# Kernel tuning notes

Hardware: AMD Instinct MI355X
Metric: run time of the kernel (lower is better)

The kernel has to match this reference:

```python
import jax, jax.numpy as jnp
import numpy as np

B = 4096          # number of sessions
MEAN_LEN = 50     # mean items per session
N = B * MEAN_LEN  # total items (ragged lengths sum to this)
H = 256           # feat_input_dim == context_input_dim == hidden_dim


def setup_inputs() -> dict:
    key = jax.random.key(0)
    k1, k2, k3, k4, k5, k6, k7 = jax.random.split(key, 7)
    # ragged lengths in [20, 80] adjusted so they sum exactly to N
    rng = np.random.default_rng(0)
    lens = rng.integers(20, 81, size=B)
    lens = (lens * (N / lens.sum())).astype(np.int64)
    lens[-1] += N - lens.sum()
    s = 1.0 / np.sqrt(H)
    return {
        "feats": jax.random.normal(k1, (N, H), jnp.float32),
        "feat_context": jax.random.normal(k2, (N, H), jnp.float32),
        "batch_num_items": jnp.asarray(lens, jnp.int64),
        "Wu": jax.random.uniform(k3, (H, H), jnp.float32, -s, s),
        "bu": jax.random.uniform(k4, (H,), jnp.float32, -s, s),
        "Wv": jax.random.uniform(k5, (H, H), jnp.float32, -s, s),
        "We": jax.random.uniform(k6, (H,), jnp.float32, -s, s),
        "Wout": jax.random.uniform(k7, (H, H), jnp.float32, -s, s),
    }


def reference(feats, feat_context, batch_num_items, Wu, bu, Wv, We, Wout):
    n = feats.shape[0]
    b = batch_num_items.shape[0]
    # additive attention score per item
    feat_u = feats @ Wu.T + bu                     # [N, H]
    feat_v = feat_context @ Wv.T                   # [N, H]
    e = jax.nn.sigmoid(feat_u + feat_v) @ We       # [N]
    # segment ids from ragged lengths (static total length => jit-safe)
    seg = jnp.repeat(jnp.arange(b), batch_num_items, total_repeat_length=n)
    # segment softmax (numerically stable)
    m = jax.ops.segment_max(e, seg, num_segments=b)        # [B]
    ex = jnp.exp(e - m[seg])                               # [N]
    denom = jax.ops.segment_sum(ex, seg, num_segments=b)   # [B]
    alpha = ex / denom[seg]                                # [N]
    # weighted segment-sum pooling
    rst = jax.ops.segment_sum(feats * alpha[:, None], seg, num_segments=b)  # [B, H]
    return rst @ Wout.T
```

## Files before the change

### kernel.cpp

```cpp
#include <hip/hip_runtime.h>
#include <hip/hip_bf16.h>
#include <cstdint>
#include <cstddef>

#define H 256
#define CHUNK 128

typedef __attribute__((ext_vector_type(8))) short    frag8;
typedef __attribute__((ext_vector_type(4))) float    f32x4;
typedef __attribute__((ext_vector_type(4))) uint32_t u32x4;
typedef __attribute__((ext_vector_type(8))) unsigned short ushort8;

__device__ __forceinline__ unsigned short f32_to_bf16(float f) {
    uint32_t u = __float_as_uint(f);
    u = (u + 0x7FFFu + ((u >> 16) & 1u)) >> 16;
    return (unsigned short)u;
}

__device__ __forceinline__ uint32_t pk_bf16(float a, float b) {
    union { __hip_bfloat162 h2; uint32_t u; } cv;
    cv.h2 = __float22bfloat162_rn(make_float2(a, b));
    return cv.u;
}

__global__ void prep(const float* __restrict__ Wu, const float* __restrict__ Wv,
                     const float* __restrict__ Wout,
                     unsigned short* __restrict__ Wopt, float* __restrict__ WoutT) {
    int bid = blockIdx.x, tid = threadIdx.x;
    if (bid < 64) {
        int idx  = bid * 256 + tid;
        int lane = idx & 63;
        int ct   = (idx >> 6) & 15;
        int ksg  = idx >> 10;
        int col  = ct * 16 + (lane & 15);
        int kg   = ksg * 32 + (lane >> 4) * 8;
        ushort8 pk;
        #pragma unroll
        for (int j = 0; j < 8; j++) {
            int k = kg + j;
            float v = (k < 256) ? Wu[col * 256 + k] : Wv[col * 256 + (k - 256)];
            pk[j] = f32_to_bf16(v);
        }
        *(ushort8*)&Wopt[(size_t)idx * 8] = pk;
    } else {
        int t2 = (bid - 64) * 256 + tid;
        int j = t2 & 255, k = t2 >> 8;
        WoutT[t2] = Wout[j * 256 + k];
    }
}

__global__ void seg_offsets(const int* __restrict__ lens, int B, int* __restrict__ off,
                            int2* __restrict__ chunks, int* __restrict__ chunk_cnt) {
    __shared__ int partL[256], partC[256];
    int tid = threadIdx.x;
    bool is64 = (B >= 3) && (lens[1] == 0) && (lens[3] == 0) && (lens[5] == 0);
    int per = (B + 255) / 256;
    int base = tid * per;
    int sL = 0, sC = 0;
    for (int i = 0; i < per; i++) {
        int idx = base + i;
        if (idx < B) {
            int l = is64 ? lens[2 * idx] : lens[idx];
            sL += l;
            sC += (l + CHUNK - 1) / CHUNK;
        }
    }
    partL[tid] = sL; partC[tid] = sC;
    __syncthreads();
    for (int d = 1; d < 256; d <<= 1) {
        int vL = partL[tid], vC = partC[tid];
        int aL = (tid >= d) ? partL[tid - d] : 0;
        int aC = (tid >= d) ? partC[tid - d] : 0;
        __syncthreads();
        partL[tid] = vL + aL; partC[tid] = vC + aC;
        __syncthreads();
    }
    int runL = partL[tid] - sL;
    int runC = partC[tid] - sC;
    for (int i = 0; i < per; i++) {
        int idx = base + i;
        if (idx < B) {
            int l = is64 ? lens[2 * idx] : lens[idx];
            off[idx] = runL;
            int n = (l + CHUNK - 1) / CHUNK;
            for (int c = 0; c < n; c++)
                chunks[runC + c] = make_int2(idx, runL + c * CHUNK);
            runC += n;
            runL += l;
        }
    }
    if (tid == 255) { off[B] = partL[255]; chunk_cnt[0] = partC[255]; }
}

__global__ __launch_bounds__(512, 4) void fused_e(
        const float* __restrict__ feats, const float* __restrict__ ctx,
        const unsigned short* __restrict__ Wopt,
        const float* __restrict__ bu, const float* __restrict__ We,
        float* __restrict__ e_out) {
    __shared__ unsigned short a_lds[64 * 128];
    __shared__ float e_part[8 * 64];

    const int tid  = threadIdx.x;
    const int lane = tid & 63;
    const int w    = tid >> 6;
    const int l15  = lane & 15;
    const int q    = lane >> 4;
    const size_t m0 = (size_t)blockIdx.x * 64;
    const int r0   = tid >> 3;
    const int c8   = tid & 7;
    const int swz  = r0 & 15;

    f32x4 acc[4][2];
    #pragma unroll
    for (int i = 0; i < 4; i++)
        #pragma unroll
        for (int j = 0; j < 2; j++)
            acc[i][j] = (f32x4)(0.0f);

    f32x4 pre[4];
    {
        const float* p = feats + (m0 + r0) * H + c8 * 16;
        pre[0] = *(const f32x4*)p;       pre[1] = *(const f32x4*)(p + 4);
        pre[2] = *(const f32x4*)(p + 8); pre[3] = *(const f32x4*)(p + 12);
    }

    #pragma unroll
    for (int kt = 0; kt < 4; ++kt) {
        u32x4 g0, g1;
        g0[0] = pk_bf16(pre[0][0], pre[0][1]); g0[1] = pk_bf16(pre[0][2], pre[0][3]);
        g0[2] = pk_bf16(pre[1][0], pre[1][1]); g0[3] = pk_bf16(pre[1][2], pre[1][3]);
        g1[0] = pk_bf16(pre[2][0], pre[2][1]); g1[1] = pk_bf16(pre[2][2], pre[2][3]);
        g1[2] = pk_bf16(pre[3][0], pre[3][1]); g1[3] = pk_bf16(pre[3][2], pre[3][3]);

        __syncthreads();
        *(u32x4*)&a_lds[r0 * 128 + (((2 * c8    ) ^ swz) * 8)] = g0;
        *(u32x4*)&a_lds[r0 * 128 + (((2 * c8 + 1) ^ swz) * 8)] = g1;
        __syncthreads();

        frag8 bfr[4][2];
        #pragma unroll
        for (int ks = 0; ks < 4; ++ks)
            #pragma unroll
            for (int ci = 0; ci < 2; ++ci)
                bfr[ks][ci] = *(const frag8*)&Wopt[
                    (((size_t)(kt * 4 + ks) * 16 + (w * 2 + ci)) * 64 + lane) * 8];
        __builtin_amdgcn_sched_barrier(0);

        if (kt < 3) {
            const float* src = (kt + 1 < 2) ? feats : ctx;
            const int kb = ((kt + 1) & 1) * 128;
            const float* p = src + (m0 + r0) * H + kb + c8 * 16;
            pre[0] = *(const f32x4*)p;       pre[1] = *(const f32x4*)(p + 4);
            pre[2] = *(const f32x4*)(p + 8); pre[3] = *(const f32x4*)(p + 12);
        }

        #pragma unroll
        for (int ks = 0; ks < 4; ++ks) {
            frag8 afr[4];
            #pragma unroll
            for (int rt = 0; rt < 4; ++rt)
                afr[rt] = *(const frag8*)&a_lds[(rt * 16 + l15) * 128 + (((ks * 4 + q) ^ l15) * 8)];
            #pragma unroll
            for (int rt = 0; rt < 4; ++rt)
                #pragma unroll
                for (int ci = 0; ci < 2; ++ci)
                    acc[rt][ci] = __builtin_amdgcn_mfma_f32_16x16x32_bf16(
                        afr[rt], bfr[ks][ci], acc[rt][ci], 0, 0, 0);
        }
    }

    float buv[2], wev[2];
    #pragma unroll
    for (int ci = 0; ci < 2; ++ci) {
        int col = w * 32 + ci * 16 + l15;
        buv[ci] = bu[col];
        wev[ci] = We[col];
    }
    #pragma unroll
    for (int rt = 0; rt < 4; ++rt) {
        #pragma unroll
        for (int r = 0; r < 4; ++r) {
            float s = 0.0f;
            #pragma unroll
            for (int ci = 0; ci < 2; ++ci) {
                float h = acc[rt][ci][r] + buv[ci];
                s += wev[ci] * __builtin_amdgcn_rcpf(1.0f + __expf(-h));
            }
            s += __shfl_xor(s, 1, 64);
            s += __shfl_xor(s, 2, 64);
            s += __shfl_xor(s, 4, 64);
            s += __shfl_xor(s, 8, 64);
            if (l15 == 0) e_part[w * 64 + rt * 16 + q * 4 + r] = s;
        }
    }
    __syncthreads();
    if (tid < 64) {
        float s = 0.0f;
        #pragma unroll
        for (int ww = 0; ww < 8; ++ww) s += e_part[ww * 64 + tid];
        e_out[m0 + tid] = s;
    }
}

__global__ __launch_bounds__(256) void seg_stats(
        float* __restrict__ e, const int* __restrict__ off, int B) {
    int seg = blockIdx.x * 4 + (threadIdx.x >> 6);
    int lane = threadIdx.x & 63;
    if (seg >= B) return;
    int start = off[seg];
    int len = off[seg + 1] - start;
    float m = -3.0e38f;
    for (int i = lane; i < len; i += 64) m = fmaxf(m, e[start + i]);
    #pragma unroll
    for (int o = 32; o > 0; o >>= 1) m = fmaxf(m, __shfl_xor(m, o, 64));
    float s = 0.0f;
    for (int i = lane; i < len; i += 64) s += __expf(e[start + i] - m);
    #pragma unroll
    for (int o = 32; o > 0; o >>= 1) s += __shfl_xor(s, o, 64);
    float inv = (s > 0.0f) ? 1.0f / s : 0.0f;
    for (int i = lane; i < len; i += 64) e[start + i] = __expf(e[start + i] - m) * inv;
}

__global__ __launch_bounds__(256) void pool_chunks(
        const float* __restrict__ alpha, const float* __restrict__ feats,
        const int* __restrict__ off, const int2* __restrict__ chunks,
        const int* __restrict__ chunk_cnt, float* __restrict__ rst) {
    __shared__ float redf[4 * 256];
    int idx = blockIdx.x;
    if (idx >= chunk_cnt[0]) return;
    int2 en = chunks[idx];
    int seg = en.x, cstart = en.y;
    int sstart = off[seg], send = off[seg + 1];
    int clen = send - cstart;
    if (clen > CHUNK) clen = CHUNK;
    int tid = threadIdx.x, lane = tid & 63, g = tid >> 6;

    const f32x4* F = (const f32x4*)feats + (size_t)cstart * 64 + lane;
    const float* A = alpha + cstart;
    f32x4 acc0 = (f32x4)(0.0f), acc1 = (f32x4)(0.0f);
    int i = g;
    for (; i + 4 < clen; i += 8) {
        acc0 += A[i]     * F[(size_t)i * 64];
        acc1 += A[i + 4] * F[(size_t)(i + 4) * 64];
    }
    if (i < clen) acc0 += A[i] * F[(size_t)i * 64];
    acc0 += acc1;
    *(f32x4*)&redf[g * 256 + lane * 4] = acc0;
    __syncthreads();
    float v = redf[tid] + redf[256 + tid] + redf[512 + tid] + redf[768 + tid];
    if (send - sstart > CHUNK) atomicAdd(&rst[(size_t)seg * H + tid], v);
    else rst[(size_t)seg * H + tid] = v;
}

#define RB 8
__global__ __launch_bounds__(256) void out_gemm(
        const float* __restrict__ rst, const float* __restrict__ WoutT,
        float* __restrict__ out) {
    __shared__ float r[RB * 256];
    const int tid = threadIdx.x;
    const size_t b0 = (size_t)blockIdx.x * RB;
    for (int i = tid; i < RB * 256; i += 256) r[i] = rst[b0 * 256 + i];
    __syncthreads();
    float acc[RB];
    #pragma unroll
    for (int j = 0; j < RB; j++) acc[j] = 0.0f;
    for (int k = 0; k < 256; k += 4) {
        f32x4 rw[RB];
        #pragma unroll
        for (int j = 0; j < RB; j++) rw[j] = *(const f32x4*)&r[j * 256 + k];
        #pragma unroll
        for (int kk = 0; kk < 4; kk++) {
            float wv = WoutT[(size_t)(k + kk) * 256 + tid];
            #pragma unroll
            for (int j = 0; j < RB; j++) acc[j] += rw[j][kk] * wv;
        }
    }
    #pragma unroll
    for (int j = 0; j < RB; j++) out[(b0 + j) * 256 + tid] = acc[j];
}

extern "C" void kernel_launch(void* const* d_in, const int* in_sizes, int n_in,
                              void* d_out, int out_size, void* d_ws, size_t ws_size,
                              hipStream_t stream) {
    const float* feats = (const float*)d_in[0];
    const float* ctx   = (const float*)d_in[1];
    const int*   lens  = (const int*)d_in[2];
    const float* Wu    = (const float*)d_in[3];
    const float* bu    = (const float*)d_in[4];
    const float* Wv    = (const float*)d_in[5];
    const float* We    = (const float*)d_in[6];
    const float* Wout  = (const float*)d_in[7];
    float* out = (float*)d_out;

    const int N = in_sizes[0] / H;
    const int B = in_sizes[2];
    const int maxChunks = B + (N + CHUNK - 1) / CHUNK;

    char* w = (char*)d_ws;
    auto carve = [&](size_t bytes) {
        char* p = w;
        w += (bytes + 255) & ~(size_t)255;
        return p;
    };
    int*            off    = (int*)           carve((size_t)(B + 1) * sizeof(int));
    float*          e      = (float*)         carve((size_t)N * sizeof(float));
    float*          rst    = (float*)         carve((size_t)B * H * sizeof(float));
    unsigned short* Wopt   = (unsigned short*)carve((size_t)16 * 16 * 64 * 8 * sizeof(unsigned short));
    float*          WoutT  = (float*)         carve((size_t)H * H * sizeof(float));
    int2*           chunks = (int2*)          carve((size_t)maxChunks * sizeof(int2));
    int*            ccnt   = (int*)           carve(sizeof(int));

    hipMemsetAsync(rst, 0, (size_t)B * H * sizeof(float), stream);

    prep        <<<320,         256, 0, stream>>>(Wu, Wv, Wout, Wopt, WoutT);
    seg_offsets <<<1,           256, 0, stream>>>(lens, B, off, chunks, ccnt);
    fused_e     <<<N / 64,      512, 0, stream>>>(feats, ctx, Wopt, bu, We, e);
    seg_stats   <<<(B + 3) / 4, 256, 0, stream>>>(e, off, B);
    pool_chunks <<<maxChunks,   256, 0, stream>>>(e, feats, off, chunks, ccnt, rst);
    out_gemm    <<<B / RB,      256, 0, stream>>>(rst, WoutT, out);
}
```

Measured before the change: 525.4 us.

## Persistent double-buffered fused_e kernel and fuse segment softmax into pooling

Measured after the change: 583.7 us. 11.1% more time.

```diff
diff --git a/kernel.cpp b/kernel.cpp
--- a/kernel.cpp
+++ b/kernel.cpp
@@ -96,8 +96,8 @@
         const float* __restrict__ feats, const float* __restrict__ ctx,
         const unsigned short* __restrict__ Wopt,
         const float* __restrict__ bu, const float* __restrict__ We,
-        float* __restrict__ e_out) {
-    __shared__ unsigned short a_lds[64 * 128];
+        float* __restrict__ e_out, int nTiles) {
+    __shared__ unsigned short a_lds[2][64 * 128];
     __shared__ float e_part[8 * 64];
 
     const int tid  = threadIdx.x;
@@ -105,10 +105,20 @@
     const int w    = tid >> 6;
     const int l15  = lane & 15;
     const int q    = lane >> 4;
-    const size_t m0 = (size_t)blockIdx.x * 64;
     const int r0   = tid >> 3;
     const int c8   = tid & 7;
     const int swz  = r0 & 15;
+    const int G    = gridDim.x;
+
+    if (blockIdx.x >= nTiles) return;
+
+    float buv[2], wev[2];
+    #pragma unroll
+    for (int ci = 0; ci < 2; ++ci) {
+        int col = w * 32 + ci * 16 + l15;
+        buv[ci] = bu[col];
+        wev[ci] = We[col];
+    }
 
     f32x4 acc[4][2];
     #pragma unroll
@@ -118,87 +128,90 @@
             acc[i][j] = (f32x4)(0.0f);
 
     f32x4 pre[4];
-    {
-        const float* p = feats + (m0 + r0) * H + c8 * 16;
+    auto loadA = [&](int tile, int kt) {
+        const float* s = (kt < 2) ? feats : ctx;
+        const float* p = s + ((size_t)tile * 64 + r0) * H + ((kt & 1) << 7) + (c8 << 4);
         pre[0] = *(const f32x4*)p;       pre[1] = *(const f32x4*)(p + 4);
         pre[2] = *(const f32x4*)(p + 8); pre[3] = *(const f32x4*)(p + 12);
-    }
-
-    #pragma unroll
-    for (int kt = 0; kt < 4; ++kt) {
+    };
+    auto cvt_store = [&](int buf) {
         u32x4 g0, g1;
         g0[0] = pk_bf16(pre[0][0], pre[0][1]); g0[1] = pk_bf16(pre[0][2], pre[0][3]);
         g0[2] = pk_bf16(pre[1][0], pre[1][1]); g0[3] = pk_bf16(pre[1][2], pre[1][3]);
         g1[0] = pk_bf16(pre[2][0], pre[2][1]); g1[1] = pk_bf16(pre[2][2], pre[2][3]);
         g1[2] = pk_bf16(pre[3][0], pre[3][1]); g1[3] = pk_bf16(pre[3][2], pre[3][3]);
-
-        __syncthreads();
-        *(u32x4*)&a_lds[r0 * 128 + (((2 * c8    ) ^ swz) * 8)] = g0;
-        *(u32x4*)&a_lds[r0 * 128 + (((2 * c8 + 1) ^ swz) * 8)] = g1;
-        __syncthreads();
-
-        frag8 bfr[4][2];
-        #pragma unroll
-        for (int ks = 0; ks < 4; ++ks)
-            #pragma unroll
-            for (int ci = 0; ci < 2; ++ci)
-                bfr[ks][ci] = *(const frag8*)&Wopt[
-                    (((size_t)(kt * 4 + ks) * 16 + (w * 2 + ci)) * 64 + lane) * 8];
-        __builtin_amdgcn_sched_barrier(0);
-
-        if (kt < 3) {
-            const float* src = (kt + 1 < 2) ? feats : ctx;
-            const int kb = ((kt + 1) & 1) * 128;
-            const float* p = src + (m0 + r0) * H + kb + c8 * 16;
-            pre[0] = *(const f32x4*)p;       pre[1] = *(const f32x4*)(p + 4);
-            pre[2] = *(const f32x4*)(p + 8); pre[3] = *(const f32x4*)(p + 12);
-        }
-
-        #pragma unroll
-        for (int ks = 0; ks < 4; ++ks) {
-            frag8 afr[4];
-            #pragma unroll
-            for (int rt = 0; rt < 4; ++rt)
-                afr[rt] = *(const frag8*)&a_lds[(rt * 16 + l15) * 128 + (((ks * 4 + q) ^ l15) * 8)];
-            #pragma unroll
-            for (int rt = 0; rt < 4; ++rt)
+        *(u32x4*)&a_lds[buf][r0 * 128 + (((2 * c8    ) ^ swz) * 8)] = g0;
+        *(u32x4*)&a_lds[buf][r0 * 128 + (((2 * c8 + 1) ^ swz) * 8)] = g1;
+    };
+
+    loadA(blockIdx.x, 0);
+    cvt_store(0);
+    loadA(blockIdx.x, 1);
+    __syncthreads();
+
+    int cur = 0;
+    for (int tile = blockIdx.x; tile < nTiles; tile += G) {
+        #pragma unroll
+        for (int kt = 0; kt < 4; ++kt) {
+            frag8 bfr[4][2];
+            #pragma unroll
+            for (int ks = 0; ks < 4; ++ks)
                 #pragma unroll
                 for (int ci = 0; ci < 2; ++ci)
-                    acc[rt][ci] = __builtin_amdgcn_mfma_f32_16x16x32_bf16(
-                        afr[rt], bfr[ks][ci], acc[rt][ci], 0, 0, 0);
-        }
-    }
-
-    float buv[2], wev[2];
-    #pragma unroll
-    for (int ci = 0; ci < 2; ++ci) {
-        int col = w * 32 + ci * 16 + l15;
-        buv[ci] = bu[col];
-        wev[ci] = We[col];
-    }
-    #pragma unroll
-    for (int rt = 0; rt < 4; ++rt) {
-        #pragma unroll
-        for (int r = 0; r < 4; ++r) {
+                    bfr[ks][ci] = *(const frag8*)&Wopt[
+                        (((size_t)(kt * 4 + ks) * 16 + (w * 2 + ci)) * 64 + lane) * 8];
+
+            #pragma unroll
+            for (int ks = 0; ks < 4; ++ks) {
+                frag8 afr[4];
+                #pragma unroll
+                for (int rt = 0; rt < 4; ++rt)
+                    afr[rt] = *(const frag8*)&a_lds[cur][(rt * 16 + l15) * 128 + (((ks * 4 + q) ^ l15) * 8)];
+                #pragma unroll
+                for (int rt = 0; rt < 4; ++rt)
+                    #pragma unroll
+                    for (int ci = 0; ci < 2; ++ci)
+                        acc[rt][ci] = __builtin_amdgcn_mfma_f32_16x16x32_bf16(
+                            afr[rt], bfr[ks][ci], acc[rt][ci], 0, 0, 0);
+            }
+
+            const bool last_step = (kt == 3) && (tile + G >= nTiles);
+            if (!last_step) {
+                cvt_store(cur ^ 1);
+                int kt2 = kt + 2, tile2 = tile;
+                if (kt2 >= 4) { kt2 -= 4; tile2 += G; }
+                if (tile2 < nTiles) loadA(tile2, kt2);
+            }
+            cur ^= 1;
+            __syncthreads();
+        }
+
+        #pragma unroll
+        for (int rt = 0; rt < 4; ++rt) {
+            #pragma unroll
+            for (int r = 0; r < 4; ++r) {
+                float s = 0.0f;
+                #pragma unroll
+                for (int ci = 0; ci < 2; ++ci) {
+                    float h = acc[rt][ci][r] + buv[ci];
+                    s += wev[ci] * __builtin_amdgcn_rcpf(1.0f + __expf(-h));
+                    acc[rt][ci][r] = 0.0f;
+                }
+                s += __shfl_xor(s, 1, 64);
+                s += __shfl_xor(s, 2, 64);
+                s += __shfl_xor(s, 4, 64);
+                s += __shfl_xor(s, 8, 64);
+                if (l15 == 0) e_part[w * 64 + rt * 16 + q * 4 + r] = s;
+            }
+        }
+        __syncthreads();
+        if (tid < 64) {
             float s = 0.0f;
             #pragma unroll
-            for (int ci = 0; ci < 2; ++ci) {
-                float h = acc[rt][ci][r] + buv[ci];
-                s += wev[ci] * __builtin_amdgcn_rcpf(1.0f + __expf(-h));
-            }
-            s += __shfl_xor(s, 1, 64);
-            s += __shfl_xor(s, 2, 64);
-            s += __shfl_xor(s, 4, 64);
-            s += __shfl_xor(s, 8, 64);
-            if (l15 == 0) e_part[w * 64 + rt * 16 + q * 4 + r] = s;
-        }
-    }
-    __syncthreads();
-    if (tid < 64) {
-        float s = 0.0f;
-        #pragma unroll
-        for (int ww = 0; ww < 8; ++ww) s += e_part[ww * 64 + tid];
-        e_out[m0 + tid] = s;
+            for (int ww = 0; ww < 8; ++ww) s += e_part[ww * 64 + tid];
+            e_out[(size_t)tile * 64 + tid] = s;
+        }
+        __syncthreads();
     }
 }
 
@@ -209,6 +222,7 @@
     if (seg >= B) return;
     int start = off[seg];
     int len = off[seg + 1] - start;
+    if (len <= CHUNK) return;
     float m = -3.0e38f;
     for (int i = lane; i < len; i += 64) m = fmaxf(m, e[start + i]);
     #pragma unroll
@@ -222,10 +236,11 @@
 }
 
 __global__ __launch_bounds__(256) void pool_chunks(
-        const float* __restrict__ alpha, const float* __restrict__ feats,
+        const float* __restrict__ ealpha, const float* __restrict__ feats,
         const int* __restrict__ off, const int2* __restrict__ chunks,
         const int* __restrict__ chunk_cnt, float* __restrict__ rst) {
     __shared__ float redf[4 * 256];
+    __shared__ float smred[8];
     int idx = blockIdx.x;
     if (idx >= chunk_cnt[0]) return;
     int2 en = chunks[idx];
@@ -234,21 +249,45 @@
     int clen = send - cstart;
     if (clen > CHUNK) clen = CHUNK;
     int tid = threadIdx.x, lane = tid & 63, g = tid >> 6;
+    const bool multi = (send - sstart) > CHUNK;
+
+    float m = 0.0f, inv = 1.0f;
+    if (!multi) {
+        float v = (tid < clen) ? ealpha[cstart + tid] : -3.0e38f;
+        #pragma unroll
+        for (int o = 32; o > 0; o >>= 1) v = fmaxf(v, __shfl_xor(v, o, 64));
+        if (lane == 0) smred[g] = v;
+        __syncthreads();
+        m = fmaxf(fmaxf(smred[0], smred[1]), fmaxf(smred[2], smred[3]));
+        float x = (tid < clen) ? __expf(ealpha[cstart + tid] - m) : 0.0f;
+        #pragma unroll
+        for (int o = 32; o > 0; o >>= 1) x += __shfl_xor(x, o, 64);
+        if (lane == 0) smred[4 + g] = x;
+        __syncthreads();
+        float ssum = smred[4] + smred[5] + smred[6] + smred[7];
+        inv = (ssum > 0.0f) ? 1.0f / ssum : 0.0f;
+    }
 
     const f32x4* F = (const f32x4*)feats + (size_t)cstart * 64 + lane;
-    const float* A = alpha + cstart;
+    const float* A = ealpha + cstart;
     f32x4 acc0 = (f32x4)(0.0f), acc1 = (f32x4)(0.0f);
     int i = g;
     for (; i + 4 < clen; i += 8) {
-        acc0 += A[i]     * F[(size_t)i * 64];
-        acc1 += A[i + 4] * F[(size_t)(i + 4) * 64];
-    }
-    if (i < clen) acc0 += A[i] * F[(size_t)i * 64];
+        float w0 = A[i], w1 = A[i + 4];
+        if (!multi) { w0 = __expf(w0 - m) * inv; w1 = __expf(w1 - m) * inv; }
+        acc0 += w0 * F[(size_t)i * 64];
+        acc1 += w1 * F[(size_t)(i + 4) * 64];
+    }
+    if (i < clen) {
+        float w0 = A[i];
+        if (!multi) w0 = __expf(w0 - m) * inv;
+        acc0 += w0 * F[(size_t)i * 64];
+    }
     acc0 += acc1;
     *(f32x4*)&redf[g * 256 + lane * 4] = acc0;
     __syncthreads();
     float v = redf[tid] + redf[256 + tid] + redf[512 + tid] + redf[768 + tid];
-    if (send - sstart > CHUNK) atomicAdd(&rst[(size_t)seg * H + tid], v);
+    if (multi) atomicAdd(&rst[(size_t)seg * H + tid], v);
     else rst[(size_t)seg * H + tid] = v;
 }
 
@@ -295,6 +334,7 @@
     const int N = in_sizes[0] / H;
     const int B = in_sizes[2];
     const int maxChunks = B + (N + CHUNK - 1) / CHUNK;
+    const int nTiles = N / 64;
 
     char* w = (char*)d_ws;
     auto carve = [&](size_t bytes) {
@@ -312,9 +352,11 @@
 
     hipMemsetAsync(rst, 0, (size_t)B * H * sizeof(float), stream);
 
+    const int gE = (nTiles < 512) ? nTiles : 512;
+
     prep        <<<320,         256, 0, stream>>>(Wu, Wv, Wout, Wopt, WoutT);
     seg_offsets <<<1,           256, 0, stream>>>(lens, B, off, chunks, ccnt);
-    fused_e     <<<N / 64,      512, 0, stream>>>(feats, ctx, Wopt, bu, We, e);
+    fused_e     <<<gE,          512, 0, stream>>>(feats, ctx, Wopt, bu, We, e, nTiles);
     seg_stats   <<<(B + 3) / 4, 256, 0, stream>>>(e, off, B);
     pool_chunks <<<maxChunks,   256, 0, stream>>>(e, feats, off, chunks, ccnt, rst);
     out_gemm    <<<B / RB,      256, 0, stream>>>(rst, WoutT, out);
```
